# Performance work log

Hardware: AMD Instinct MI355X
Metric: run time of the kernel (lower is better)

Reference implementation:

```python
import jax, jax.numpy as jnp
import numpy as np

UNITS = 512
GROUPS = 32
EPS = 1e-3  # keras GroupNormalization default epsilon


def group_norm(x, gamma, beta):
    # x: [B,H,W,C]; normalize over (H,W, channels-within-group)
    B, H, W, C = x.shape
    xg = x.reshape(B, H, W, GROUPS, C // GROUPS)
    mean = xg.mean(axis=(1, 2, 4), keepdims=True)
    var = xg.var(axis=(1, 2, 4), keepdims=True)
    xn = (xg - mean) * jax.lax.rsqrt(var + EPS)
    return xn.reshape(B, H, W, C) * gamma + beta


def setup_inputs() -> dict:
    key = jax.random.key(0)
    ks = jax.random.split(key, 6)
    B, H, W, C = 16, 32, 32, UNITS
    std = 0.02  # RandomNormal(stddev=0.02) kernel init
    return {
        "x": jax.random.normal(ks[0], (B, H, W, C), jnp.float32),
        "gamma": jnp.ones((C,), jnp.float32),
        "beta": jnp.zeros((C,), jnp.float32),
        "Wq": std * jax.random.normal(ks[1], (C, UNITS), jnp.float32),
        "bq": jnp.zeros((UNITS,), jnp.float32),
        "Wk": std * jax.random.normal(ks[2], (C, UNITS), jnp.float32),
        "bk": jnp.zeros((UNITS,), jnp.float32),
        "Wv": std * jax.random.normal(ks[3], (C, UNITS), jnp.float32),
        "bv": jnp.zeros((UNITS,), jnp.float32),
        "Wp": std * jax.random.normal(ks[4], (UNITS, UNITS), jnp.float32),
        "bp": jnp.zeros((UNITS,), jnp.float32),
    }


def reference(x, gamma, beta, Wq, bq, Wk, bk, Wv, bv, Wp, bp):
    B, H, W, C = x.shape
    scale = jnp.float32(UNITS) ** -0.5
    xn = group_norm(x, gamma, beta)  # note: original residual uses normalized input
    # flatten spatial dims to N = H*W tokens (same math as bhwc/bHWc einsums)
    xf = xn.reshape(B, H * W, C)
    q = xf @ Wq + bq
    k = xf @ Wk + bk
    v = xf @ Wv + bv
    scores = jnp.einsum('bnc,bmc->bnm', q, k) * scale  # [B, N, N]
    attn = jax.nn.softmax(scores, axis=-1)
    out = jnp.einsum('bnm,bmc->bnc', attn, v)
    proj = out @ Wp + bp
    return xn + proj.reshape(B, H, W, C)
```

## Files before the change

### kernel.cpp

```cpp
#include <hip/hip_runtime.h>
#include <math.h>

#define BATCH 16
#define NTOK  1024
#define CH    512
#define NGRP  32
#define GSZ   16
#define EPSV  1e-3f
#define MTOT  (BATCH*NTOK)
#define SCALE 0.04419417382415922f
#define SEXP  (SCALE*1.4426950408889634f)

typedef unsigned short u16;
typedef __attribute__((ext_vector_type(4))) float f32x4;
typedef __attribute__((ext_vector_type(8))) short s16x8;

__device__ __forceinline__ u16 f2bf(float f) {
    union { float f; unsigned u; } x{f};
    unsigned r = x.u + 0x7fff + ((x.u >> 16) & 1);
    return (u16)(r >> 16);
}

__device__ __forceinline__ void gld16(const u16* g, u16* l) {
    __builtin_amdgcn_global_load_lds(
        (const __attribute__((address_space(1))) void*)g,
        (__attribute__((address_space(3))) void*)l, 16, 0, 0);
}

#define MFMA16 __builtin_amdgcn_mfma_f32_16x16x32_bf16

__global__ __launch_bounds__(256) void gn_stats(const float* __restrict__ x,
                                                float2* __restrict__ stats) {
    int bg = blockIdx.x;
    int b = bg >> 5, g = bg & 31;
    const float* base = x + (size_t)b * NTOK * CH + g * GSZ;
    float s = 0.f, ss = 0.f;
    for (int i = threadIdx.x; i < 4096; i += 256) {
        int p = i >> 2, c4 = i & 3;
        float4 v = *(const float4*)(base + (size_t)p * CH + c4 * 4);
        s  += v.x + v.y + v.z + v.w;
        ss += v.x * v.x + v.y * v.y + v.z * v.z + v.w * v.w;
    }
    for (int off = 32; off; off >>= 1) {
        s  += __shfl_down(s, off);
        ss += __shfl_down(ss, off);
    }
    __shared__ float2 part[4];
    if ((threadIdx.x & 63) == 0) part[threadIdx.x >> 6] = make_float2(s, ss);
    __syncthreads();
    if (threadIdx.x == 0) {
        float S = 0.f, SS = 0.f;
        for (int i = 0; i < 4; i++) { S += part[i].x; SS += part[i].y; }
        float mean = S * (1.f / 16384.f);
        float var  = SS * (1.f / 16384.f) - mean * mean;
        stats[bg] = make_float2(mean, rsqrtf(var + EPSV));
    }
}

__global__ __launch_bounds__(256) void gn_apply(const float* __restrict__ x,
                                                const float2* __restrict__ stats,
                                                const float* __restrict__ gamma,
                                                const float* __restrict__ beta,
                                                float* __restrict__ xn,
                                                u16* __restrict__ xnb) {
    size_t total = (size_t)MTOT * CH / 4;
    for (size_t i4 = (size_t)blockIdx.x * 256 + threadIdx.x; i4 < total;
         i4 += (size_t)gridDim.x * 256) {
        size_t flat = i4 * 4;
        int c = (int)(flat & (CH - 1));
        int b = (int)(flat >> 19);
        int g = c >> 4;
        float2 st = stats[(b << 5) + g];
        float4 xv = *(const float4*)(x + flat);
        float4 gv = *(const float4*)(gamma + c);
        float4 bv = *(const float4*)(beta + c);
        float4 o;
        o.x = (xv.x - st.x) * st.y * gv.x + bv.x;
        o.y = (xv.y - st.x) * st.y * gv.y + bv.y;
        o.z = (xv.z - st.x) * st.y * gv.z + bv.z;
        o.w = (xv.w - st.x) * st.y * gv.w + bv.w;
        *(float4*)(xn + flat) = o;
        uint2 h;
        h.x = (unsigned)f2bf(o.x) | ((unsigned)f2bf(o.y) << 16);
        h.y = (unsigned)f2bf(o.z) | ((unsigned)f2bf(o.w) << 16);
        *(uint2*)(xnb + flat) = h;
    }
}

__global__ __launch_bounds__(256) void weights_prep(
    const float* __restrict__ Wq, const float* __restrict__ Wk,
    const float* __restrict__ Wv, const float* __restrict__ Wp,
    u16* __restrict__ WTqkv, u16* __restrict__ WTp) {
    int z = blockIdx.z;
    const float* src = z == 0 ? Wq : z == 1 ? Wk : z == 2 ? Wv : Wp;
    u16* dst = z < 3 ? WTqkv + (size_t)z * CH * CH : WTp;
    __shared__ u16 tile[64][66];
    int r0 = blockIdx.y * 64, c0 = blockIdx.x * 64;
    int t = threadIdx.x;
    for (int i = 0; i < 16; i++) {
        int idx = i * 256 + t;
        int r = idx >> 6, c = idx & 63;
        tile[r][c] = f2bf(src[(size_t)(r0 + r) * CH + c0 + c]);
    }
    __syncthreads();
    for (int i = 0; i < 16; i++) {
        int idx = i * 256 + t;
        int oc = idx >> 6, orr = idx & 63;
        dst[(size_t)(c0 + oc) * CH + r0 + orr] = tile[orr][oc];
    }
}

__global__ void prep_bias(const float* __restrict__ bq, const float* __restrict__ bk,
                          const float* __restrict__ bv, float* __restrict__ bqkv) {
    int t = blockIdx.x * 256 + threadIdx.x;
    bqkv[t] = t < 512 ? bq[t] : (t < 1024 ? bk[t - 512] : bv[t - 1024]);
}

__global__ __launch_bounds__(256) void vt_transpose(const u16* __restrict__ in,
                                                    u16* __restrict__ out,
                                                    int R, int C, int ldIn,
                                                    long sIn, long sOut) {
    __shared__ u16 tile[64][66];
    int z = blockIdx.z;
    in  += (size_t)z * sIn;
    out += (size_t)z * sOut;
    int r0 = blockIdx.y * 64, c0 = blockIdx.x * 64;
    int t = threadIdx.x;
    for (int i = 0; i < 16; i++) {
        int idx = i * 256 + t;
        int r = idx >> 6, c = idx & 63;
        tile[r][c] = in[(size_t)(r0 + r) * ldIn + c0 + c];
    }
    __syncthreads();
    for (int i = 0; i < 16; i++) {
        int idx = i * 256 + t;
        int oc = idx >> 6, orr = idx & 63;
        out[(size_t)(c0 + oc) * R + r0 + orr] = tile[orr][oc];
    }
}

template <bool BIAS, bool RES, bool OUTF32>
__global__ __launch_bounds__(256) void gemm_bt(
    const u16* __restrict__ A, const u16* __restrict__ B, void* __restrict__ Cout,
    const float* __restrict__ bias, const float* __restrict__ res,
    int K, int lda, int ldb, int ldc,
    long sA, long sB, long sC, float alpha) {
    __shared__ __align__(16) u16 Asm[8192];
    __shared__ __align__(16) u16 Bsm[8192];

    unsigned flat = blockIdx.x + gridDim.x * (blockIdx.y + gridDim.y * blockIdx.z);
    unsigned nb = gridDim.x * gridDim.y * gridDim.z;
    unsigned lf = (flat & 7) * (nb >> 3) + (flat >> 3);
    unsigned pb = gridDim.x * gridDim.y;
    unsigned bz = lf / pb, rem = lf - bz * pb;
    unsigned by = rem / gridDim.x, bx = rem - by * gridDim.x;

    A += (size_t)bz * sA;
    B += (size_t)bz * sB;
    size_t zc = (size_t)bz * sC;

    int t = threadIdx.x;
    int wave = t >> 6, lane = t & 63;
    int wm = wave >> 1, wn = wave & 1;
    int rowA0 = by * 128;
    int colB0 = bx * 128;

    int c16log = (lane & 3) ^ ((lane >> 3) & 3);
    const u16* aG[2]; const u16* bG[2]; u16* aL[2]; u16* bL[2];
#pragma unroll
    for (int j = 0; j < 2; j++) {
        int s = wave * 2 + j;
        int row = s * 16 + (lane >> 2);
        aL[j] = Asm + s * 512;
        bL[j] = Bsm + s * 512;
        aG[j] = A + (size_t)(rowA0 + row) * lda + c16log * 8;
        bG[j] = B + (size_t)(colB0 + row) * ldb + c16log * 8;
    }

    int kg = lane >> 4;
    int aoff[4], boff[4];
#pragma unroll
    for (int i = 0; i < 4; i++) {
        int ra = wm * 64 + i * 16 + (lane & 15);
        aoff[i] = ra * 32 + (kg ^ ((ra >> 1) & 3)) * 8;
        int rb = wn * 64 + i * 16 + (lane & 15);
        boff[i] = rb * 32 + (kg ^ ((rb >> 1) & 3)) * 8;
    }

#define STG_G(buf, ktE)                          \
    {                                            \
        gld16(aG[0] + (ktE), aL[0] + (buf) * 4096); \
        gld16(aG[1] + (ktE), aL[1] + (buf) * 4096); \
        gld16(bG[0] + (ktE), bL[0] + (buf) * 4096); \
        gld16(bG[1] + (ktE), bL[1] + (buf) * 4096); \
    }

    f32x4 acc[4][4] = {};
    int nk = K >> 5;
    STG_G(0, 0);
    __syncthreads();
    for (int kt = 0; kt < nk; kt++) {
        if (kt + 1 < nk) STG_G((kt + 1) & 1, (kt + 1) * 32);
        const u16* as = Asm + (kt & 1) * 4096;
        const u16* bs = Bsm + (kt & 1) * 4096;
        s16x8 af[4], bfr[4];
#pragma unroll
        for (int i = 0; i < 4; i++) {
            af[i]  = *(const s16x8*)(as + aoff[i]);
            bfr[i] = *(const s16x8*)(bs + boff[i]);
        }
#pragma unroll
        for (int mi = 0; mi < 4; mi++)
#pragma unroll
            for (int nj = 0; nj < 4; nj++)
                acc[mi][nj] = MFMA16(af[mi], bfr[nj], acc[mi][nj], 0, 0, 0);
        __syncthreads();
    }
#undef STG_G

    int r0 = rowA0 + wm * 64 + (lane >> 4) * 4;
    int c0c = colB0 + wn * 64 + (lane & 15);
#pragma unroll
    for (int mi = 0; mi < 4; mi++) {
#pragma unroll
        for (int nj = 0; nj < 4; nj++) {
            int c = c0c + nj * 16;
            float bv = BIAS ? bias[c] : 0.f;
            f32x4 v = acc[mi][nj];
#pragma unroll
            for (int j = 0; j < 4; j++) {
                int rr = r0 + mi * 16 + j;
                float val = v[j] * alpha + bv;
                if (RES) val += res[(size_t)rr * ldc + c];
                if (OUTF32) ((float*)Cout)[zc + (size_t)rr * ldc + c] = val;
                else        ((u16*)Cout)[zc + (size_t)rr * ldc + c] = f2bf(val);
            }
        }
    }
}

__global__ __launch_bounds__(512) void attn_fused(const u16* __restrict__ qkv,
                                                  const u16* __restrict__ vtg,
                                                  u16* __restrict__ ao) {
    __shared__ __align__(16) u16 S[65536];

    unsigned flat = blockIdx.x;
    unsigned lf = (flat & 7) * 32 + (flat >> 3);
    int b = lf >> 4, mt = lf & 15;

    int t = threadIdx.x, w = t >> 6, lane = t & 63;
    int rt = w >> 2, ct = w & 3;
    int l15 = lane & 15, kg = lane >> 4;

    const u16* kbase = qkv + (size_t)b * NTOK * 1536 + CH;
    int c16log = (lane & 3) ^ ((lane >> 3) & 3);

    const u16* bG[8];
#pragma unroll
    for (int j = 0; j < 8; j++) {
        int row = (w * 8 + j) * 16 + (lane >> 2);
        bG[j] = kbase + (size_t)row * 1536 + c16log * 8;
    }
    const u16* qp[2];
#pragma unroll
    for (int rg = 0; rg < 2; rg++)
        qp[rg] = qkv + (size_t)(b * NTOK + mt * 64 + rt * 32 + rg * 16 + l15) * 1536 + kg * 8;

    int rbb = ct * 256 + l15;
    int boffb = rbb * 32 + ((kg ^ ((rbb >> 1) & 3)) << 3);

    f32x4 acc1[2][16];
#pragma unroll
    for (int rg = 0; rg < 2; rg++)
#pragma unroll
        for (int nj = 0; nj < 16; nj++) acc1[rg][nj] = f32x4{0.f, 0.f, 0.f, 0.f};

#define KSTG(buf, kt)                                                        \
    { _Pragma("unroll")                                                      \
      for (int j = 0; j < 8; j++)                                            \
          gld16(bG[j] + (kt) * 32, S + (buf) * 32768 + (w * 8 + j) * 512); }

    KSTG(0, 0);
    s16x8 aqc[2], aqn[2];
    aqc[0] = *(const s16x8*)(qp[0]);
    aqc[1] = *(const s16x8*)(qp[1]);
    __syncthreads();
#pragma unroll
    for (int kt = 0; kt < 16; kt++) {
        if (kt < 15) {
            KSTG((kt + 1) & 1, kt + 1);
            aqn[0] = *(const s16x8*)(qp[0] + (kt + 1) * 32);
            aqn[1] = *(const s16x8*)(qp[1] + (kt + 1) * 32);
        }
        const u16* bb = S + (kt & 1) * 32768;
#pragma unroll
        for (int nj = 0; nj < 16; nj++) {
            s16x8 bf = *(const s16x8*)(bb + boffb + nj * 512);
            acc1[0][nj] = MFMA16(aqc[0], bf, acc1[0][nj], 0, 0, 0);
            acc1[1][nj] = MFMA16(aqc[1], bf, acc1[1][nj], 0, 0, 0);
        }
        if (kt < 15) { aqc[0] = aqn[0]; aqc[1] = aqn[1]; }
        __syncthreads();
    }
#undef KSTG

    float* redm = (float*)S;
    float* reds = redm + 256;
    float mr[2][4], iv[2][4];
#pragma unroll
    for (int rg = 0; rg < 2; rg++)
#pragma unroll
        for (int j = 0; j < 4; j++) {
            float m = acc1[rg][0][j];
#pragma unroll
            for (int nj = 1; nj < 16; nj++) m = fmaxf(m, acc1[rg][nj][j]);
            for (int off = 1; off < 16; off <<= 1) m = fmaxf(m, __shfl_xor(m, off));
            mr[rg][j] = m;
        }
    if (l15 == 0) {
#pragma unroll
        for (int rg = 0; rg < 2; rg++)
#pragma unroll
            for (int j = 0; j < 4; j++)
                redm[(rt * 32 + rg * 16 + kg * 4 + j) * 4 + ct] = mr[rg][j];
    }
    __syncthreads();
#pragma unroll
    for (int rg = 0; rg < 2; rg++)
#pragma unroll
        for (int j = 0; j < 4; j++) {
            int row = rt * 32 + rg * 16 + kg * 4 + j;
            mr[rg][j] = fmaxf(fmaxf(redm[row * 4], redm[row * 4 + 1]),
                              fmaxf(redm[row * 4 + 2], redm[row * 4 + 3]));
        }
#pragma unroll
    for (int rg = 0; rg < 2; rg++)
#pragma unroll
        for (int j = 0; j < 4; j++) {
            float s = 0.f;
#pragma unroll
            for (int nj = 0; nj < 16; nj++) {
                float e = exp2f((acc1[rg][nj][j] - mr[rg][j]) * SEXP);
                acc1[rg][nj][j] = e;
                s += e;
            }
            for (int off = 1; off < 16; off <<= 1) s += __shfl_xor(s, off);
            if (l15 == 0) reds[(rt * 32 + rg * 16 + kg * 4 + j) * 4 + ct] = s;
        }
    __syncthreads();
#pragma unroll
    for (int rg = 0; rg < 2; rg++)
#pragma unroll
        for (int j = 0; j < 4; j++) {
            int row = rt * 32 + rg * 16 + kg * 4 + j;
            iv[rg][j] = 1.f / (reds[row * 4] + reds[row * 4 + 1] +
                               reds[row * 4 + 2] + reds[row * 4 + 3]);
        }
    __syncthreads();

    const u16* vG[4];
#pragma unroll
    for (int sj = 0; sj < 4; sj++) {
        int chrow = (w * 4 + sj) * 16 + (lane >> 2);
        vG[sj] = vtg + ((size_t)b * 512 + chrow) * 1024 + c16log * 8;
    }
#define VSTG(buf, hf, c)                                                     \
    { _Pragma("unroll")                                                      \
      for (int sj = 0; sj < 4; sj++)                                         \
          gld16(vG[sj] + (hf) * 512 + (c) * 32,                              \
                S + 32768 + (buf) * 16384 + (w * 4 + sj) * 512); }

    f32x4 acc2[2][8];
#pragma unroll
    for (int rg = 0; rg < 2; rg++)
#pragma unroll
        for (int cj = 0; cj < 8; cj++) acc2[rg][cj] = f32x4{0.f, 0.f, 0.f, 0.f};

    int prow[2] = {rt * 32 + l15, rt * 32 + 16 + l15};
    int chl = ct * 128 + l15;
    int voffb = chl * 32 + ((kg ^ ((chl >> 1) & 3)) << 3);

    for (int hf = 0; hf < 2; hf++) {
        VSTG(0, hf, 0);
        if ((ct >> 1) == hf) {
            int kb16 = (ct & 1) * 256;
#pragma unroll
            for (int rg = 0; rg < 2; rg++)
#pragma unroll
                for (int nj = 0; nj < 16; nj++) {
                    int klocal = kb16 + nj * 16 + l15;
                    int g = klocal >> 3, ko = klocal & 7;
#pragma unroll
                    for (int j = 0; j < 4; j++) {
                        int row = rt * 32 + rg * 16 + kg * 4 + j;
                        S[row * 512 + (((g ^ (row & 7))) << 3) + ko] =
                            f2bf(acc1[rg][nj][j] * iv[rg][j]);
                    }
                }
        }
        __syncthreads();
        for (int c = 0; c < 16; c++) {
            if (c < 15) VSTG((c + 1) & 1, hf, c + 1);
            const u16* vb = S + 32768 + (c & 1) * 16384;
            s16x8 pa[2];
#pragma unroll
            for (int rg = 0; rg < 2; rg++) {
                int row = prow[rg];
                pa[rg] = *(const s16x8*)(S + row * 512 + (((c * 4 + kg) ^ (row & 7)) << 3));
            }
#pragma unroll
            for (int cj = 0; cj < 8; cj++) {
                s16x8 vf = *(const s16x8*)(vb + voffb + cj * 512);
                acc2[0][cj] = MFMA16(pa[0], vf, acc2[0][cj], 0, 0, 0);
                acc2[1][cj] = MFMA16(pa[1], vf, acc2[1][cj], 0, 0, 0);
            }
            __syncthreads();
        }
    }
#undef VSTG

#pragma unroll
    for (int rg = 0; rg < 2; rg++)
#pragma unroll
        for (int cj = 0; cj < 8; cj++)
#pragma unroll
            for (int j = 0; j < 4; j++) {
                int row = rt * 32 + rg * 16 + kg * 4 + j;
                int ch = ct * 128 + cj * 16 + l15;
                S[row * 512 + ((((ch >> 3) ^ (row & 7))) << 3) + (ch & 7)] =
                    f2bf(acc2[rg][cj][j]);
            }
    __syncthreads();
    u16* aop = ao + (size_t)(b * NTOK + mt * 64) * 512;
#pragma unroll
    for (int i = 0; i < 8; i++) {
        int f = i * 512 + t;
        int row = f >> 6, g = f & 63;
        uint4 v = *(const uint4*)(S + row * 512 + g * 8);
        *(uint4*)(aop + (size_t)row * 512 + ((g ^ (row & 7)) << 3)) = v;
    }
}

extern "C" void kernel_launch(void* const* d_in, const int* in_sizes, int n_in,
                              void* d_out, int out_size, void* d_ws, size_t ws_size,
                              hipStream_t stream) {
    const float* x     = (const float*)d_in[0];
    const float* gamma = (const float*)d_in[1];
    const float* beta  = (const float*)d_in[2];
    const float* Wq    = (const float*)d_in[3];
    const float* bq    = (const float*)d_in[4];
    const float* Wk    = (const float*)d_in[5];
    const float* bk    = (const float*)d_in[6];
    const float* Wv    = (const float*)d_in[7];
    const float* bv    = (const float*)d_in[8];
    const float* Wp    = (const float*)d_in[9];
    const float* bp    = (const float*)d_in[10];
    float* out = (float*)d_out;

    const size_t SZ  = (size_t)MTOT * CH;
    const size_t NSZ = (size_t)NTOK * CH;

    char* p = (char*)d_ws;
    float*  xn    = (float*)p;   p += SZ * 4;
    u16*    xnb   = (u16*)p;     p += SZ * 2;
    u16*    qkvb  = (u16*)p;     p += (size_t)MTOT * 3 * CH * 2;
    u16*    vt    = (u16*)p;     p += SZ * 2;
    u16*    ao    = (u16*)p;     p += SZ * 2;
    u16*    WTqkv = (u16*)p;     p += (size_t)3 * CH * CH * 2;
    u16*    WTp   = (u16*)p;     p += (size_t)CH * CH * 2;
    float*  bqkv  = (float*)p;   p += 3 * CH * 4;
    float2* stats = (float2*)p;

    dim3 blk(256);

    gn_stats<<<BATCH * NGRP, blk, 0, stream>>>(x, stats);
    gn_apply<<<2048, blk, 0, stream>>>(x, stats, gamma, beta, xn, xnb);
    weights_prep<<<dim3(8, 8, 4), blk, 0, stream>>>(Wq, Wk, Wv, Wp, WTqkv, WTp);
    prep_bias<<<6, blk, 0, stream>>>(bq, bk, bv, bqkv);

    gemm_bt<true, false, false><<<dim3(12, 128, 1), blk, 0, stream>>>(
        xnb, WTqkv, qkvb, bqkv, nullptr, CH, CH, CH, 3 * CH, 0, 0, 0, 1.f);

    vt_transpose<<<dim3(8, 16, BATCH), blk, 0, stream>>>(
        qkvb + 2 * CH, vt, NTOK, CH, 3 * CH, (long)NTOK * 3 * CH, (long)NSZ);

    attn_fused<<<256, 512, 0, stream>>>(qkvb, vt, ao);

    gemm_bt<true, true, true><<<dim3(4, 128, 1), blk, 0, stream>>>(
        ao, WTp, out, bp, xn, CH, CH, CH, CH, 0, 0, 0, 1.f);
}
```

Before: 307.8 us.

## Write full P tile to LDS and read V directly from global in PV loop

The PV stage no longer runs two halves with double-buffered V tiles staged into LDS through global_load_lds. It writes the whole normalized 64x1024 probability tile into shared memory once, then streams V fragments straight from global memory into registers, with no per-chunk barriers. The launch bounds now also request two blocks per CU. This cuts LDS staging and synchronisation, but makes each MFMA depend on global-load latency with no explicit prefetch, and the occupancy hint may force register spills. The 128 KB LDS tile may also prevent two blocks from actually fitting on a CU.

```diff
diff --git a/kernel.cpp b/kernel.cpp
--- a/kernel.cpp
+++ b/kernel.cpp
@@ -239,9 +239,9 @@
     }
 }
 
-__global__ __launch_bounds__(512) void attn_fused(const u16* __restrict__ qkv,
-                                                  const u16* __restrict__ vtg,
-                                                  u16* __restrict__ ao) {
+__global__ __launch_bounds__(512, 2) void attn_fused(const u16* __restrict__ qkv,
+                                                     const u16* __restrict__ vtg,
+                                                     u16* __restrict__ ao) {
     __shared__ __align__(16) u16 S[65536];
 
     unsigned flat = blockIdx.x;
@@ -358,17 +358,20 @@
         }
     __syncthreads();
 
-    const u16* vG[4];
-#pragma unroll
-    for (int sj = 0; sj < 4; sj++) {
-        int chrow = (w * 4 + sj) * 16 + (lane >> 2);
-        vG[sj] = vtg + ((size_t)b * 512 + chrow) * 1024 + c16log * 8;
-    }
-#define VSTG(buf, hf, c)                                                     \
-    { _Pragma("unroll")                                                      \
-      for (int sj = 0; sj < 4; sj++)                                         \
-          gld16(vG[sj] + (hf) * 512 + (c) * 32,                              \
-                S + 32768 + (buf) * 16384 + (w * 4 + sj) * 512); }
+#pragma unroll
+    for (int rg = 0; rg < 2; rg++)
+#pragma unroll
+        for (int nj = 0; nj < 16; nj++) {
+            int k = ct * 256 + nj * 16 + l15;
+            int g = k >> 3, ko = k & 7;
+#pragma unroll
+            for (int j = 0; j < 4; j++) {
+                int row = rt * 32 + rg * 16 + kg * 4 + j;
+                S[row * 1024 + ((g ^ (row & 7)) << 3) + ko] =
+                    f2bf(acc1[rg][nj][j] * iv[rg][j]);
+            }
+        }
+    __syncthreads();
 
     f32x4 acc2[2][8];
 #pragma unroll
@@ -376,49 +379,28 @@
 #pragma unroll
         for (int cj = 0; cj < 8; cj++) acc2[rg][cj] = f32x4{0.f, 0.f, 0.f, 0.f};
 
-    int prow[2] = {rt * 32 + l15, rt * 32 + 16 + l15};
-    int chl = ct * 128 + l15;
-    int voffb = chl * 32 + ((kg ^ ((chl >> 1) & 3)) << 3);
-
-    for (int hf = 0; hf < 2; hf++) {
-        VSTG(0, hf, 0);
-        if ((ct >> 1) == hf) {
-            int kb16 = (ct & 1) * 256;
-#pragma unroll
-            for (int rg = 0; rg < 2; rg++)
-#pragma unroll
-                for (int nj = 0; nj < 16; nj++) {
-                    int klocal = kb16 + nj * 16 + l15;
-                    int g = klocal >> 3, ko = klocal & 7;
-#pragma unroll
-                    for (int j = 0; j < 4; j++) {
-                        int row = rt * 32 + rg * 16 + kg * 4 + j;
-                        S[row * 512 + (((g ^ (row & 7))) << 3) + ko] =
-                            f2bf(acc1[rg][nj][j] * iv[rg][j]);
-                    }
-                }
-        }
-        __syncthreads();
-        for (int c = 0; c < 16; c++) {
-            if (c < 15) VSTG((c + 1) & 1, hf, c + 1);
-            const u16* vb = S + 32768 + (c & 1) * 16384;
-            s16x8 pa[2];
-#pragma unroll
-            for (int rg = 0; rg < 2; rg++) {
-                int row = prow[rg];
-                pa[rg] = *(const s16x8*)(S + row * 512 + (((c * 4 + kg) ^ (row & 7)) << 3));
-            }
-#pragma unroll
-            for (int cj = 0; cj < 8; cj++) {
-                s16x8 vf = *(const s16x8*)(vb + voffb + cj * 512);
-                acc2[0][cj] = MFMA16(pa[0], vf, acc2[0][cj], 0, 0, 0);
-                acc2[1][cj] = MFMA16(pa[1], vf, acc2[1][cj], 0, 0, 0);
-            }
-            __syncthreads();
-        }
-    }
-#undef VSTG
-
+    const u16* vrow[8];
+#pragma unroll
+    for (int cj = 0; cj < 8; cj++)
+        vrow[cj] = vtg + ((size_t)b * 512 + ct * 128 + cj * 16 + l15) * 1024 + kg * 8;
+
+    int prowA[2] = {rt * 32 + l15, rt * 32 + 16 + l15};
+    for (int c = 0; c < 32; c++) {
+        s16x8 pa[2];
+#pragma unroll
+        for (int rg = 0; rg < 2; rg++) {
+            int row = prowA[rg];
+            pa[rg] = *(const s16x8*)(S + row * 1024 + (((c * 4 + kg) ^ (row & 7)) << 3));
+        }
+#pragma unroll
+        for (int cj = 0; cj < 8; cj++) {
+            s16x8 vf = *(const s16x8*)(vrow[cj] + c * 32);
+            acc2[0][cj] = MFMA16(pa[0], vf, acc2[0][cj], 0, 0, 0);
+            acc2[1][cj] = MFMA16(pa[1], vf, acc2[1][cj], 0, 0, 0);
+        }
+    }
+
+    __syncthreads();
 #pragma unroll
     for (int rg = 0; rg < 2; rg++)
 #pragma unroll
```

Measured after the change: 283.2 us. 1.09x faster.
